# Performance work log

Measured on AMD Instinct MI355X. Metric: run time of the kernel, lower is better.

Reference implementation:

```python
import jax, jax.numpy as jnp
import numpy as np

B, CIN, COUT = 8, 16, 16
D = H = W = 48
M1 = M2 = M3 = 12


def dht3(x):
    # Discrete Hartley Transform over the last three (spatial) dims:
    # DHT(x) = Re(FFT(x)) - Im(FFT(x))
    X = jnp.fft.fftn(x, axes=(-3, -2, -1))
    return X.real - X.imag


def flip_periodic(x):
    # Faithful to the torch code: flatten the last 3 dims, keep element 0,
    # reverse the remainder, reshape back. (NOT a per-axis flip.)
    shape = x.shape
    xf = x.reshape(shape[:-3] + (-1,))
    z = jnp.concatenate([xf[..., :1], xf[..., 1:][..., ::-1]], axis=-1)
    return z.reshape(shape)


def setup_inputs() -> dict:
    key = jax.random.key(0)
    k1, k2 = jax.random.split(key)
    x = jax.random.normal(k1, (B, CIN, D, H, W), dtype=jnp.float32)
    # constant error -> max-min <= 1e-8 -> normalized_error = 0 -> full modes used
    error_signal = jnp.zeros((B, D, H, W), dtype=jnp.float32)
    scale = 1.0 / (CIN * COUT)
    weights = scale * jax.random.uniform(k2, (CIN, COUT, M1, M2, M3), dtype=jnp.float32)
    return {"x": x, "error_signal": error_signal, "weights": weights}


def reference(x, error_signal, weights):
    # Single region covering the whole volume (region_size == size, overlap 0).
    # Zero-pad the low-mode weight block to the full region size.
    Cin, Cout, m1, m2, m3 = weights.shape
    d, h, w = x.shape[2:]
    kernel = jnp.zeros((Cin, Cout, d, h, w), dtype=x.dtype)
    kernel = kernel.at[:, :, :m1, :m2, :m3].set(weights)

    X = dht3(x)            # [b, i, d, h, w]
    Y = dht3(kernel)       # [i, o, d, h, w]
    Xflip = flip_periodic(X)
    Yflip = flip_periodic(Y)
    Yeven = 0.5 * (Y + Yflip)
    Yodd = 0.5 * (Y - Yflip)
    Z = (jnp.einsum('bixyz,ioxyz->boxyz', X, Yeven)
         + jnp.einsum('bixyz,ioxyz->boxyz', Xflip, Yodd))
    # IDHT: DHT is involutory -> idht(Z) = dht(Z) / n
    n = d * h * w
    out = dht3(Z) / n
    # overlap_counts is 1 everywhere for a single region -> division is identity
    return out
```

## Files before the change

kernel.cpp:

```cpp
#include <hip/hip_runtime.h>

#define NVOL   110592
#define PLANE  2304
#define TWO_PI 6.28318530717958647692f

__device__ __forceinline__ float dot4(float4 a, float4 b, float acc) {
    acc = fmaf(a.x, b.x, acc); acc = fmaf(a.y, b.y, acc);
    acc = fmaf(a.z, b.z, acc); acc = fmaf(a.w, b.w, acc);
    return acc;
}
__device__ __forceinline__ float dot4m(float4 a, float4 b, float acc) {
    acc = fmaf(-a.x, b.x, acc); acc = fmaf(-a.y, b.y, acc);
    acc = fmaf(-a.z, b.z, acc); acc = fmaf(-a.w, b.w, acc);
    return acc;
}

template<int LH, int LW>
__global__ void __launch_bounds__(192) cas_wh_kernel(const float* __restrict__ in,
                                                     float* __restrict__ out,
                                                     size_t inVol, size_t inPlane, int inRow,
                                                     size_t outVol, size_t outPlane) {
    __shared__ float cas48[48];
    __shared__ __align__(16) float casT[2304];
    __shared__ __align__(16) float tile[LH][48];
    __shared__ __align__(16) float tmp[LH * 48];
    const int tid = threadIdx.x;
    const int d = blockIdx.x, v = blockIdx.y;

    if (tid < 48) { float ang = (float)tid * (TWO_PI / 48.0f); cas48[tid] = cosf(ang) + sinf(ang); }
    __syncthreads();
    for (int idx = tid; idx < 2304; idx += 192) {
        int j = idx / 48, k = idx % 48;
        casT[idx] = cas48[(j * k) % 48];
    }
    const float* ib = in + (size_t)v * inVol + (size_t)d * inPlane;
    for (int idx = tid; idx < LH * LW; idx += 192)
        tile[idx / LW][idx % LW] = ib[(idx / LW) * inRow + (idx % LW)];
    __syncthreads();

    const float4* casT4 = reinterpret_cast<const float4*>(casT);
    float4* tmp4 = reinterpret_cast<float4*>(tmp);
    for (int o4 = tid; o4 < LH * 12; o4 += 192) {
        int h = o4 / 12, kq = o4 % 12;
        float4 acc = make_float4(0.f, 0.f, 0.f, 0.f);
        #pragma unroll 4
        for (int j = 0; j < LW; ++j) {
            float  t = tile[h][j];
            float4 c = casT4[j * 12 + kq];
            acc.x = fmaf(t, c.x, acc.x); acc.y = fmaf(t, c.y, acc.y);
            acc.z = fmaf(t, c.z, acc.z); acc.w = fmaf(t, c.w, acc.w);
        }
        tmp4[o4] = acc;
    }
    __syncthreads();
    float4* ob = reinterpret_cast<float4*>(out + (size_t)v * outVol + (size_t)d * outPlane);
    for (int o4 = tid; o4 < 576; o4 += 192) {
        int kh = o4 / 12, wq = o4 % 12;
        float4 acc = make_float4(0.f, 0.f, 0.f, 0.f);
        #pragma unroll 4
        for (int j = 0; j < LH; ++j) {
            float  c = casT[j * 48 + kh];
            float4 t = tmp4[j * 12 + wq];
            acc.x = fmaf(t.x, c, acc.x); acc.y = fmaf(t.y, c, acc.y);
            acc.z = fmaf(t.z, c, acc.z); acc.w = fmaf(t.w, c, acc.w);
        }
        ob[o4] = acc;
    }
}

__global__ void __launch_bounds__(192) cas_wh48(const float* __restrict__ in,
                                                float* __restrict__ out) {
    __shared__ float cas48[48];
    __shared__ __align__(16) float casT[2304];
    __shared__ __align__(16) float buf[4][2496];
    const int tid = threadIdx.x;
    const int bx = blockIdx.x, v = blockIdx.y;

    if (tid < 48) { float ang = (float)tid * (TWO_PI / 48.0f); cas48[tid] = cosf(ang) + sinf(ang); }
    __syncthreads();
    for (int idx = tid; idx < 2304; idx += 192) {
        int j = idx / 48, k = idx % 48;
        casT[idx] = cas48[(j * k) % 48];
    }
    const float* ib = in + (size_t)v * NVOL + (size_t)(bx * 4) * PLANE;
    for (int idx = tid; idx < 2304; idx += 192) {
        int p = idx / 576, r = idx % 576, h = r / 12, q = r % 12;
        float4 t = *reinterpret_cast<const float4*>(ib + (size_t)p * PLANE + h * 48 + q * 4);
        float* dst = &buf[p][h * 49 + q * 4];
        dst[0] = t.x; dst[1] = t.y; dst[2] = t.z; dst[3] = t.w;
    }
    __syncthreads();

    const int p = tid / 48, pp = tid % 48;
    const int hg = pp >> 2, kg = pp & 3;
    float* tile = buf[p];
    const float4* casT4 = reinterpret_cast<const float4*>(casT);

    float4 acc[4][3];
    #pragma unroll
    for (int i = 0; i < 4; ++i)
        #pragma unroll
        for (int q = 0; q < 3; ++q) acc[i][q] = make_float4(0.f, 0.f, 0.f, 0.f);

    #pragma unroll 4
    for (int j = 0; j < 48; ++j) {
        float t0 = tile[(hg * 4 + 0) * 49 + j];
        float t1 = tile[(hg * 4 + 1) * 49 + j];
        float t2 = tile[(hg * 4 + 2) * 49 + j];
        float t3 = tile[(hg * 4 + 3) * 49 + j];
        float4 c[3];
        #pragma unroll
        for (int q = 0; q < 3; ++q) c[q] = casT4[j * 12 + kg * 3 + q];
        #pragma unroll
        for (int q = 0; q < 3; ++q) {
            acc[0][q].x = fmaf(t0, c[q].x, acc[0][q].x); acc[0][q].y = fmaf(t0, c[q].y, acc[0][q].y);
            acc[0][q].z = fmaf(t0, c[q].z, acc[0][q].z); acc[0][q].w = fmaf(t0, c[q].w, acc[0][q].w);
            acc[1][q].x = fmaf(t1, c[q].x, acc[1][q].x); acc[1][q].y = fmaf(t1, c[q].y, acc[1][q].y);
            acc[1][q].z = fmaf(t1, c[q].z, acc[1][q].z); acc[1][q].w = fmaf(t1, c[q].w, acc[1][q].w);
            acc[2][q].x = fmaf(t2, c[q].x, acc[2][q].x); acc[2][q].y = fmaf(t2, c[q].y, acc[2][q].y);
            acc[2][q].z = fmaf(t2, c[q].z, acc[2][q].z); acc[2][q].w = fmaf(t2, c[q].w, acc[2][q].w);
            acc[3][q].x = fmaf(t3, c[q].x, acc[3][q].x); acc[3][q].y = fmaf(t3, c[q].y, acc[3][q].y);
            acc[3][q].z = fmaf(t3, c[q].z, acc[3][q].z); acc[3][q].w = fmaf(t3, c[q].w, acc[3][q].w);
        }
    }
    __syncthreads();
    float* tmp = buf[p];
    #pragma unroll
    for (int i = 0; i < 4; ++i)
        #pragma unroll
        for (int q = 0; q < 3; ++q)
            *reinterpret_cast<float4*>(&tmp[(hg * 4 + i) * 52 + kg * 12 + q * 4]) = acc[i][q];
    __syncthreads();

    float4 acc2[4][3];
    #pragma unroll
    for (int i = 0; i < 4; ++i)
        #pragma unroll
        for (int q = 0; q < 3; ++q) acc2[i][q] = make_float4(0.f, 0.f, 0.f, 0.f);

    #pragma unroll 4
    for (int h = 0; h < 48; ++h) {
        float4 cf = casT4[h * 12 + hg];
        float cfa[4] = {cf.x, cf.y, cf.z, cf.w};
        float4 m[3];
        #pragma unroll
        for (int q = 0; q < 3; ++q) m[q] = *reinterpret_cast<const float4*>(&tmp[h * 52 + kg * 12 + q * 4]);
        #pragma unroll
        for (int i = 0; i < 4; ++i)
            #pragma unroll
            for (int q = 0; q < 3; ++q) {
                acc2[i][q].x = fmaf(cfa[i], m[q].x, acc2[i][q].x);
                acc2[i][q].y = fmaf(cfa[i], m[q].y, acc2[i][q].y);
                acc2[i][q].z = fmaf(cfa[i], m[q].z, acc2[i][q].z);
                acc2[i][q].w = fmaf(cfa[i], m[q].w, acc2[i][q].w);
            }
    }
    float4* ob = reinterpret_cast<float4*>(out + (size_t)v * NVOL + (size_t)(bx * 4 + p) * PLANE);
    #pragma unroll
    for (int i = 0; i < 4; ++i)
        #pragma unroll
        for (int q = 0; q < 3; ++q)
            ob[(hg * 4 + i) * 12 + kg * 3 + q] = acc2[i][q];
}

template<int JC>
__global__ void __launch_bounds__(192) cas_dcomb2(const float* __restrict__ in,
                                                  float* __restrict__ out,
                                                  size_t inVol, size_t inPlane, float scale) {
    __shared__ float cas48[48];
    __shared__ __align__(16) float casT[2304];
    __shared__ __align__(16) float tAB[2][JC * 52];
    __shared__ __align__(16) float S[2][48 * 52];
    const int tid = threadIdx.x;
    const int hp = blockIdx.x, v = blockIdx.y;
    const int hA = hp, hB = (48 - hp) % 48;

    if (tid < 48) { float ang = (float)tid * (TWO_PI / 48.0f); cas48[tid] = cosf(ang) + sinf(ang); }
    __syncthreads();
    for (int idx = tid; idx < 2304; idx += 192) {
        int j = idx / 48, k = idx % 48;
        casT[idx] = cas48[(j * k) % 48];
    }
    for (int idx = tid; idx < 2 * JC * 12; idx += 192) {
        int mm = idx / (JC * 12), r = idx % (JC * 12);
        int d = r / 12, q = r % 12;
        int hh = mm ? hB : hA;
        float4 t = *reinterpret_cast<const float4*>(in + (size_t)v * inVol + (size_t)d * inPlane + hh * 48 + q * 4);
        *reinterpret_cast<float4*>(&tAB[mm][d * 52 + q * 4]) = t;
    }
    __syncthreads();

    const int m = tid / 96, pth = tid % 96;
    const int k1g = pth >> 2, wg = pth & 3;
    float4 acc[2][3];
    #pragma unroll
    for (int i = 0; i < 2; ++i)
        #pragma unroll
        for (int q = 0; q < 3; ++q) acc[i][q] = make_float4(0.f, 0.f, 0.f, 0.f);

    #pragma unroll 4
    for (int d = 0; d < JC; ++d) {
        float c0 = casT[d * 48 + k1g * 2 + 0];
        float c1 = casT[d * 48 + k1g * 2 + 1];
        float4 t[3];
        #pragma unroll
        for (int q = 0; q < 3; ++q) t[q] = *reinterpret_cast<const float4*>(&tAB[m][d * 52 + wg * 12 + q * 4]);
        #pragma unroll
        for (int q = 0; q < 3; ++q) {
            acc[0][q].x = fmaf(c0, t[q].x, acc[0][q].x); acc[0][q].y = fmaf(c0, t[q].y, acc[0][q].y);
            acc[0][q].z = fmaf(c0, t[q].z, acc[0][q].z); acc[0][q].w = fmaf(c0, t[q].w, acc[0][q].w);
            acc[1][q].x = fmaf(c1, t[q].x, acc[1][q].x); acc[1][q].y = fmaf(c1, t[q].y, acc[1][q].y);
            acc[1][q].z = fmaf(c1, t[q].z, acc[1][q].z); acc[1][q].w = fmaf(c1, t[q].w, acc[1][q].w);
        }
    }
    #pragma unroll
    for (int i = 0; i < 2; ++i)
        #pragma unroll
        for (int q = 0; q < 3; ++q)
            *reinterpret_cast<float4*>(&S[m][(k1g * 2 + i) * 52 + wg * 12 + q * 4]) = acc[i][q];
    __syncthreads();

    float* ob = out + (size_t)v * (size_t)NVOL;
    for (int idx = tid; idx < 4608; idx += 192) {
        int side = (idx >= 2304);
        if (side && hA == hB) continue;
        int r = side ? idx - 2304 : idx;
        int k1 = r / 48, k3 = r % 48;
        int mk1 = (48 - k1) % 48, m3 = (48 - k3) % 48;
        float val;
        if (!side)
            val = S[0][k1 * 52 + m3] + S[1][k1 * 52 + k3] + S[0][mk1 * 52 + k3] - S[1][mk1 * 52 + m3];
        else
            val = S[1][k1 * 52 + m3] + S[0][k1 * 52 + k3] + S[1][mk1 * 52 + k3] - S[0][mk1 * 52 + m3];
        int k2 = side ? hB : hA;
        ob[k1 * PLANE + k2 * 48 + k3] = scale * val;
    }
}

__global__ void __launch_bounds__(256) zmul_kernel(const float* __restrict__ X,
                                                   const float* __restrict__ Y,
                                                   float* __restrict__ Z) {
    __shared__ __align__(16) float Xp[16 * 144], Xm[16 * 144];
    __shared__ __align__(16) float Yk[16 * 272], Yf[16 * 272];
    const int tid = threadIdx.x;
    const int k0 = blockIdx.x * 16;
    const bool blk0 = (blockIdx.x == 0);

    float4 xl[2], xf0[2], xf1[2];
    #pragma unroll
    for (int it = 0; it < 2; ++it) {
        int task = it * 256 + tid;
        int c = task & 127, q = task >> 7;
        const float* xb = X + (size_t)c * NVOL;
        xl[it]  = *reinterpret_cast<const float4*>(xb + k0 + 4 * q);
        xf0[it] = *reinterpret_cast<const float4*>(xb + NVOL - k0 - 4 * q - 4);
        xf1[it] = *reinterpret_cast<const float4*>(xb + NVOL - k0 - 4 * q);
    }
    float4 yl[4], yg0[4], yg1[4];
    #pragma unroll
    for (int it = 0; it < 4; ++it) {
        int task = it * 256 + tid;
        int c = task & 255, q = task >> 8;
        const float* yb = Y + (size_t)c * NVOL;
        yl[it]  = *reinterpret_cast<const float4*>(yb + k0 + 4 * q);
        yg0[it] = *reinterpret_cast<const float4*>(yb + NVOL - k0 - 4 * q - 4);
        yg1[it] = *reinterpret_cast<const float4*>(yb + NVOL - k0 - 4 * q);
    }
    #pragma unroll
    for (int it = 0; it < 2; ++it) {
        int task = it * 256 + tid;
        int c = task & 127, q = task >> 7;
        int b = c >> 4, iq = (c & 15) >> 2, ir = c & 3;
        int base = iq * 36 + b * 4 + ir;
        float a0 = xl[it].x, a1 = xl[it].y, a2 = xl[it].z, a3 = xl[it].w;
        float f0 = xf1[it].x, f1 = xf0[it].w, f2 = xf0[it].z, f3 = xf0[it].y;
        if (blk0 && q == 0) f0 = a0;
        int r0 = (4 * q + 0) * 144 + base, r1 = (4 * q + 1) * 144 + base;
        int r2 = (4 * q + 2) * 144 + base, r3 = (4 * q + 3) * 144 + base;
        Xp[r0] = a0 + f0; Xm[r0] = a0 - f0;
        Xp[r1] = a1 + f1; Xm[r1] = a1 - f1;
        Xp[r2] = a2 + f2; Xm[r2] = a2 - f2;
        Xp[r3] = a3 + f3; Xm[r3] = a3 - f3;
    }
    #pragma unroll
    for (int it = 0; it < 4; ++it) {
        int task = it * 256 + tid;
        int c = task & 255, q = task >> 8;
        int i = c >> 4, o = c & 15, iq = i >> 2, ir = i & 3;
        int base = iq * 68 + o * 4 + ir;
        float a0 = yl[it].x, a1 = yl[it].y, a2 = yl[it].z, a3 = yl[it].w;
        float f0 = yg1[it].x, f1 = yg0[it].w, f2 = yg0[it].z, f3 = yg0[it].y;
        if (blk0 && q == 0) f0 = a0;
        int r0 = (4 * q + 0) * 272 + base, r1 = (4 * q + 1) * 272 + base;
        int r2 = (4 * q + 2) * 272 + base, r3 = (4 * q + 3) * 272 + base;
        Yk[r0] = a0; Yf[r0] = f0;
        Yk[r1] = a1; Yf[r1] = f1;
        Yk[r2] = a2; Yf[r2] = f2;
        Yk[r3] = a3; Yf[r3] = f3;
    }
    __syncthreads();

    const int side = tid >> 7;
    const int r = tid & 127;
    const int tq = r >> 5, bb = (r >> 3) & 3, oo = r & 7;
    const float4* Xp4 = reinterpret_cast<const float4*>(Xp);
    const float4* Xm4 = reinterpret_cast<const float4*>(Xm);
    const float4* Yk4 = reinterpret_cast<const float4*>(Yk);
    const float4* Yf4 = reinterpret_cast<const float4*>(Yf);

    float acc[4][2][2] = {};
    if (side == 0) {
        #pragma unroll
        for (int tt = 0; tt < 4; ++tt) {
            const int t = tq * 4 + tt;
            #pragma unroll
            for (int iq = 0; iq < 4; ++iq) {
                float4 xp0 = Xp4[t * 36 + iq * 9 + bb];
                float4 xp1 = Xp4[t * 36 + iq * 9 + bb + 4];
                float4 xm0 = Xm4[t * 36 + iq * 9 + bb];
                float4 xm1 = Xm4[t * 36 + iq * 9 + bb + 4];
                float4 y0k = Yk4[t * 68 + iq * 17 + oo];
                float4 y1k = Yk4[t * 68 + iq * 17 + oo + 8];
                float4 y0f = Yf4[t * 68 + iq * 17 + oo];
                float4 y1f = Yf4[t * 68 + iq * 17 + oo + 8];
                acc[tt][0][0] = dot4(xm0, y0f, dot4(xp0, y0k, acc[tt][0][0]));
                acc[tt][0][1] = dot4(xm0, y1f, dot4(xp0, y1k, acc[tt][0][1]));
                acc[tt][1][0] = dot4(xm1, y0f, dot4(xp1, y0k, acc[tt][1][0]));
                acc[tt][1][1] = dot4(xm1, y1f, dot4(xp1, y1k, acc[tt][1][1]));
            }
        }
        #pragma unroll
        for (int bi = 0; bi < 2; ++bi)
            #pragma unroll
            for (int oi = 0; oi < 2; ++oi) {
                int bo = (bb + bi * 4) * 16 + (oo + oi * 8);
                float4 zv = make_float4(0.5f * acc[0][bi][oi], 0.5f * acc[1][bi][oi],
                                        0.5f * acc[2][bi][oi], 0.5f * acc[3][bi][oi]);
                *reinterpret_cast<float4*>(&Z[(size_t)bo * NVOL + k0 + tq * 4]) = zv;
            }
    } else {
        #pragma unroll
        for (int tt = 0; tt < 4; ++tt) {
            const int t = tq * 4 + tt;
            #pragma unroll
            for (int iq = 0; iq < 4; ++iq) {
                float4 xp0 = Xp4[t * 36 + iq * 9 + bb];
                float4 xp1 = Xp4[t * 36 + iq * 9 + bb + 4];
                float4 xm0 = Xm4[t * 36 + iq * 9 + bb];
                float4 xm1 = Xm4[t * 36 + iq * 9 + bb + 4];
                float4 y0k = Yk4[t * 68 + iq * 17 + oo];
                float4 y1k = Yk4[t * 68 + iq * 17 + oo + 8];
                float4 y0f = Yf4[t * 68 + iq * 17 + oo];
                float4 y1f = Yf4[t * 68 + iq * 17 + oo + 8];
                acc[tt][0][0] = dot4m(xm0, y0k, dot4(xp0, y0f, acc[tt][0][0]));
                acc[tt][0][1] = dot4m(xm0, y1k, dot4(xp0, y1f, acc[tt][0][1]));
                acc[tt][1][0] = dot4m(xm1, y0k, dot4(xp1, y0f, acc[tt][1][0]));
                acc[tt][1][1] = dot4m(xm1, y1k, dot4(xp1, y1f, acc[tt][1][1]));
            }
        }
        #pragma unroll
        for (int bi = 0; bi < 2; ++bi)
            #pragma unroll
            for (int oi = 0; oi < 2; ++oi) {
                int bo = (bb + bi * 4) * 16 + (oo + oi * 8);
                #pragma unroll
                for (int tt = 0; tt < 4; ++tt) {
                    int kk = k0 + tq * 4 + tt;
                    int ka = (kk == 0) ? 0 : NVOL - kk;
                    Z[(size_t)bo * NVOL + ka] = 0.5f * acc[tt][bi][oi];
                }
            }
    }
}

__global__ void __launch_bounds__(128) zmul_self_kernel(const float* __restrict__ X,
                                                        const float* __restrict__ Y,
                                                        float* __restrict__ Z) {
    const int bo = threadIdx.x, b = bo >> 4, o = bo & 15;
    const int k = NVOL / 2;
    float acc = 0.f;
    #pragma unroll
    for (int i = 0; i < 16; ++i)
        acc += X[(size_t)(b * 16 + i) * NVOL + k] * Y[(size_t)(i * 16 + o) * NVOL + k];
    Z[(size_t)bo * NVOL + k] = acc;
}

extern "C" void kernel_launch(void* const* d_in, const int* in_sizes, int n_in,
                              void* d_out, int out_size, void* d_ws, size_t ws_size,
                              hipStream_t stream) {
    const float* x = (const float*)d_in[0];
    const float* w = (const float*)d_in[2];
    float* out = (float*)d_out;

    float* HY  = (float*)d_ws;
    float* XA  = HY + (size_t)256 * NVOL;
    float* XB  = XA + (size_t)128 * NVOL;
    float* Ywh = XB;

    cas_wh_kernel<12, 12><<<dim3(12, 256), 192, 0, stream>>>(w, Ywh, 1728, 144, 12, 27648, PLANE);
    cas_dcomb2<12><<<dim3(25, 256), 192, 0, stream>>>(Ywh, HY, 27648, PLANE, 0.5f);

    cas_wh48<<<dim3(12, 128), 192, 0, stream>>>(x, XB);
    cas_dcomb2<48><<<dim3(25, 128), 192, 0, stream>>>(XB, XA, NVOL, PLANE, 0.5f);

    zmul_kernel<<<3456, 256, 0, stream>>>(XA, HY, XB);
    zmul_self_kernel<<<1, 128, 0, stream>>>(XA, HY, XB);

    cas_wh48<<<dim3(12, 128), 192, 0, stream>>>(XB, XA);
    cas_dcomb2<48><<<dim3(25, 128), 192, 0, stream>>>(XA, out, NVOL, PLANE, 0.5f / (float)NVOL);
}
```

Before: 487.6 us.

## Shrink per-block planes and LDS in DHT kernels, coalesce zmul loads

cas_wh48 now handles 3 planes per block instead of 4, with 64 threads per plane and 3x3 register tiles. That cuts shared memory and registers and raises the grid from 12 to 16 blocks per volume. cas_dcomb2<48> reuses one shared buffer for both the input tile and the intermediate S, at the cost of an extra barrier, so more blocks can fit per CU. zmul load indexing is remapped so adjacent threads read adjacent float4s within a channel, aiming for better coalescing. The risks are less ILP per thread and more re-reads of the cas table.

```diff
diff --git a/kernel.cpp b/kernel.cpp
--- a/kernel.cpp
+++ b/kernel.cpp
@@ -72,7 +72,7 @@
                                                 float* __restrict__ out) {
     __shared__ float cas48[48];
     __shared__ __align__(16) float casT[2304];
-    __shared__ __align__(16) float buf[4][2496];
+    __shared__ __align__(16) float buf[3][2496];
     const int tid = threadIdx.x;
     const int bx = blockIdx.x, v = blockIdx.y;
 
@@ -82,8 +82,8 @@
         int j = idx / 48, k = idx % 48;
         casT[idx] = cas48[(j * k) % 48];
     }
-    const float* ib = in + (size_t)v * NVOL + (size_t)(bx * 4) * PLANE;
-    for (int idx = tid; idx < 2304; idx += 192) {
+    const float* ib = in + (size_t)v * NVOL + (size_t)(bx * 3) * PLANE;
+    for (int idx = tid; idx < 1728; idx += 192) {
         int p = idx / 576, r = idx % 576, h = r / 12, q = r % 12;
         float4 t = *reinterpret_cast<const float4*>(ib + (size_t)p * PLANE + h * 48 + q * 4);
         float* dst = &buf[p][h * 49 + q * 4];
@@ -91,23 +91,22 @@
     }
     __syncthreads();
 
-    const int p = tid / 48, pp = tid % 48;
-    const int hg = pp >> 2, kg = pp & 3;
+    const int p = tid / 64, t64 = tid % 64;
+    const int hg = t64 >> 2, kg = t64 & 3;
     float* tile = buf[p];
     const float4* casT4 = reinterpret_cast<const float4*>(casT);
 
-    float4 acc[4][3];
-    #pragma unroll
-    for (int i = 0; i < 4; ++i)
+    float4 acc[3][3];
+    #pragma unroll
+    for (int i = 0; i < 3; ++i)
         #pragma unroll
         for (int q = 0; q < 3; ++q) acc[i][q] = make_float4(0.f, 0.f, 0.f, 0.f);
 
     #pragma unroll 4
     for (int j = 0; j < 48; ++j) {
-        float t0 = tile[(hg * 4 + 0) * 49 + j];
-        float t1 = tile[(hg * 4 + 1) * 49 + j];
-        float t2 = tile[(hg * 4 + 2) * 49 + j];
-        float t3 = tile[(hg * 4 + 3) * 49 + j];
+        float t0 = tile[(hg * 3 + 0) * 49 + j];
+        float t1 = tile[(hg * 3 + 1) * 49 + j];
+        float t2 = tile[(hg * 3 + 2) * 49 + j];
         float4 c[3];
         #pragma unroll
         for (int q = 0; q < 3; ++q) c[q] = casT4[j * 12 + kg * 3 + q];
@@ -119,48 +118,48 @@
             acc[1][q].z = fmaf(t1, c[q].z, acc[1][q].z); acc[1][q].w = fmaf(t1, c[q].w, acc[1][q].w);
             acc[2][q].x = fmaf(t2, c[q].x, acc[2][q].x); acc[2][q].y = fmaf(t2, c[q].y, acc[2][q].y);
             acc[2][q].z = fmaf(t2, c[q].z, acc[2][q].z); acc[2][q].w = fmaf(t2, c[q].w, acc[2][q].w);
-            acc[3][q].x = fmaf(t3, c[q].x, acc[3][q].x); acc[3][q].y = fmaf(t3, c[q].y, acc[3][q].y);
-            acc[3][q].z = fmaf(t3, c[q].z, acc[3][q].z); acc[3][q].w = fmaf(t3, c[q].w, acc[3][q].w);
         }
     }
     __syncthreads();
     float* tmp = buf[p];
     #pragma unroll
-    for (int i = 0; i < 4; ++i)
+    for (int i = 0; i < 3; ++i)
         #pragma unroll
         for (int q = 0; q < 3; ++q)
-            *reinterpret_cast<float4*>(&tmp[(hg * 4 + i) * 52 + kg * 12 + q * 4]) = acc[i][q];
-    __syncthreads();
-
-    float4 acc2[4][3];
-    #pragma unroll
-    for (int i = 0; i < 4; ++i)
+            *reinterpret_cast<float4*>(&tmp[(hg * 3 + i) * 52 + kg * 12 + q * 4]) = acc[i][q];
+    __syncthreads();
+
+    const float4* tmp4 = reinterpret_cast<const float4*>(tmp);
+    float4 acc2[3][3];
+    #pragma unroll
+    for (int i = 0; i < 3; ++i)
         #pragma unroll
         for (int q = 0; q < 3; ++q) acc2[i][q] = make_float4(0.f, 0.f, 0.f, 0.f);
 
     #pragma unroll 4
     for (int h = 0; h < 48; ++h) {
-        float4 cf = casT4[h * 12 + hg];
-        float cfa[4] = {cf.x, cf.y, cf.z, cf.w};
+        float cf0 = casT[h * 48 + hg * 3 + 0];
+        float cf1 = casT[h * 48 + hg * 3 + 1];
+        float cf2 = casT[h * 48 + hg * 3 + 2];
         float4 m[3];
         #pragma unroll
-        for (int q = 0; q < 3; ++q) m[q] = *reinterpret_cast<const float4*>(&tmp[h * 52 + kg * 12 + q * 4]);
-        #pragma unroll
-        for (int i = 0; i < 4; ++i)
-            #pragma unroll
-            for (int q = 0; q < 3; ++q) {
-                acc2[i][q].x = fmaf(cfa[i], m[q].x, acc2[i][q].x);
-                acc2[i][q].y = fmaf(cfa[i], m[q].y, acc2[i][q].y);
-                acc2[i][q].z = fmaf(cfa[i], m[q].z, acc2[i][q].z);
-                acc2[i][q].w = fmaf(cfa[i], m[q].w, acc2[i][q].w);
-            }
-    }
-    float4* ob = reinterpret_cast<float4*>(out + (size_t)v * NVOL + (size_t)(bx * 4 + p) * PLANE);
-    #pragma unroll
-    for (int i = 0; i < 4; ++i)
+        for (int q = 0; q < 3; ++q) m[q] = tmp4[h * 13 + kg * 3 + q];
+        #pragma unroll
+        for (int q = 0; q < 3; ++q) {
+            acc2[0][q].x = fmaf(cf0, m[q].x, acc2[0][q].x); acc2[0][q].y = fmaf(cf0, m[q].y, acc2[0][q].y);
+            acc2[0][q].z = fmaf(cf0, m[q].z, acc2[0][q].z); acc2[0][q].w = fmaf(cf0, m[q].w, acc2[0][q].w);
+            acc2[1][q].x = fmaf(cf1, m[q].x, acc2[1][q].x); acc2[1][q].y = fmaf(cf1, m[q].y, acc2[1][q].y);
+            acc2[1][q].z = fmaf(cf1, m[q].z, acc2[1][q].z); acc2[1][q].w = fmaf(cf1, m[q].w, acc2[1][q].w);
+            acc2[2][q].x = fmaf(cf2, m[q].x, acc2[2][q].x); acc2[2][q].y = fmaf(cf2, m[q].y, acc2[2][q].y);
+            acc2[2][q].z = fmaf(cf2, m[q].z, acc2[2][q].z); acc2[2][q].w = fmaf(cf2, m[q].w, acc2[2][q].w);
+        }
+    }
+    float4* ob = reinterpret_cast<float4*>(out + (size_t)v * NVOL + (size_t)(bx * 3 + p) * PLANE);
+    #pragma unroll
+    for (int i = 0; i < 3; ++i)
         #pragma unroll
         for (int q = 0; q < 3; ++q)
-            ob[(hg * 4 + i) * 12 + kg * 3 + q] = acc2[i][q];
+            ob[(hg * 3 + i) * 12 + kg * 3 + q] = acc2[i][q];
 }
 
 template<int JC>
@@ -169,8 +168,12 @@
                                                   size_t inVol, size_t inPlane, float scale) {
     __shared__ float cas48[48];
     __shared__ __align__(16) float casT[2304];
-    __shared__ __align__(16) float tAB[2][JC * 52];
-    __shared__ __align__(16) float S[2][48 * 52];
+    __shared__ __align__(16) float SH[2][2496];
+    __shared__ __align__(16) float tABsep[2][(JC == 48) ? 4 : JC * 52];
+    float* tAB[2];
+    if constexpr (JC == 48) { tAB[0] = SH[0]; tAB[1] = SH[1]; }
+    else                    { tAB[0] = tABsep[0]; tAB[1] = tABsep[1]; }
+
     const int tid = threadIdx.x;
     const int hp = blockIdx.x, v = blockIdx.y;
     const int hA = hp, hB = (48 - hp) % 48;
@@ -213,11 +216,12 @@
             acc[1][q].z = fmaf(c1, t[q].z, acc[1][q].z); acc[1][q].w = fmaf(c1, t[q].w, acc[1][q].w);
         }
     }
+    __syncthreads();
     #pragma unroll
     for (int i = 0; i < 2; ++i)
         #pragma unroll
         for (int q = 0; q < 3; ++q)
-            *reinterpret_cast<float4*>(&S[m][(k1g * 2 + i) * 52 + wg * 12 + q * 4]) = acc[i][q];
+            *reinterpret_cast<float4*>(&SH[m][(k1g * 2 + i) * 52 + wg * 12 + q * 4]) = acc[i][q];
     __syncthreads();
 
     float* ob = out + (size_t)v * (size_t)NVOL;
@@ -229,9 +233,9 @@
         int mk1 = (48 - k1) % 48, m3 = (48 - k3) % 48;
         float val;
         if (!side)
-            val = S[0][k1 * 52 + m3] + S[1][k1 * 52 + k3] + S[0][mk1 * 52 + k3] - S[1][mk1 * 52 + m3];
+            val = SH[0][k1 * 52 + m3] + SH[1][k1 * 52 + k3] + SH[0][mk1 * 52 + k3] - SH[1][mk1 * 52 + m3];
         else
-            val = S[1][k1 * 52 + m3] + S[0][k1 * 52 + k3] + S[1][mk1 * 52 + k3] - S[0][mk1 * 52 + m3];
+            val = SH[1][k1 * 52 + m3] + SH[0][k1 * 52 + k3] + SH[1][mk1 * 52 + k3] - SH[0][mk1 * 52 + m3];
         int k2 = side ? hB : hA;
         ob[k1 * PLANE + k2 * 48 + k3] = scale * val;
     }
@@ -250,7 +254,7 @@
     #pragma unroll
     for (int it = 0; it < 2; ++it) {
         int task = it * 256 + tid;
-        int c = task & 127, q = task >> 7;
+        int q = task & 3, c = task >> 2;
         const float* xb = X + (size_t)c * NVOL;
         xl[it]  = *reinterpret_cast<const float4*>(xb + k0 + 4 * q);
         xf0[it] = *reinterpret_cast<const float4*>(xb + NVOL - k0 - 4 * q - 4);
@@ -260,7 +264,7 @@
     #pragma unroll
     for (int it = 0; it < 4; ++it) {
         int task = it * 256 + tid;
-        int c = task & 255, q = task >> 8;
+        int q = task & 3, c = task >> 2;
         const float* yb = Y + (size_t)c * NVOL;
         yl[it]  = *reinterpret_cast<const float4*>(yb + k0 + 4 * q);
         yg0[it] = *reinterpret_cast<const float4*>(yb + NVOL - k0 - 4 * q - 4);
@@ -269,7 +273,7 @@
     #pragma unroll
     for (int it = 0; it < 2; ++it) {
         int task = it * 256 + tid;
-        int c = task & 127, q = task >> 7;
+        int q = task & 3, c = task >> 2;
         int b = c >> 4, iq = (c & 15) >> 2, ir = c & 3;
         int base = iq * 36 + b * 4 + ir;
         float a0 = xl[it].x, a1 = xl[it].y, a2 = xl[it].z, a3 = xl[it].w;
@@ -285,7 +289,7 @@
     #pragma unroll
     for (int it = 0; it < 4; ++it) {
         int task = it * 256 + tid;
-        int c = task & 255, q = task >> 8;
+        int q = task & 3, c = task >> 2;
         int i = c >> 4, o = c & 15, iq = i >> 2, ir = i & 3;
         int base = iq * 68 + o * 4 + ir;
         float a0 = yl[it].x, a1 = yl[it].y, a2 = yl[it].z, a3 = yl[it].w;
@@ -400,12 +404,12 @@
     cas_wh_kernel<12, 12><<<dim3(12, 256), 192, 0, stream>>>(w, Ywh, 1728, 144, 12, 27648, PLANE);
     cas_dcomb2<12><<<dim3(25, 256), 192, 0, stream>>>(Ywh, HY, 27648, PLANE, 0.5f);
 
-    cas_wh48<<<dim3(12, 128), 192, 0, stream>>>(x, XB);
+    cas_wh48<<<dim3(16, 128), 192, 0, stream>>>(x, XB);
     cas_dcomb2<48><<<dim3(25, 128), 192, 0, stream>>>(XB, XA, NVOL, PLANE, 0.5f);
 
     zmul_kernel<<<3456, 256, 0, stream>>>(XA, HY, XB);
     zmul_self_kernel<<<1, 128, 0, stream>>>(XA, HY, XB);
 
-    cas_wh48<<<dim3(12, 128), 192, 0, stream>>>(XB, XA);
+    cas_wh48<<<dim3(16, 128), 192, 0, stream>>>(XB, XA);
     cas_dcomb2<48><<<dim3(25, 128), 192, 0, stream>>>(XA, out, NVOL, PLANE, 0.5f / (float)NVOL);
 }
```

New measurement: 488.0 us. No clear change (+0.1%).
